# Optimization experiments

Hardware: AMD Instinct MI355X
Metric: run time of the kernel (lower is better)

## Reference

```python
import jax, jax.numpy as jnp
import numpy as np

D = 128; H = 8; DH = D // H; L = 3
NA = 8000; NL = 32000; N = NA + NL
E1 = 65536; D_RPE = 5; D_FFN = 2 * D; RF_H = 128


def _ln(x, eps=1e-5):
    mu = x.mean(-1, keepdims=True)
    var = ((x - mu) ** 2).mean(-1, keepdims=True)
    return (x - mu) * jax.lax.rsqrt(var + eps)


def _rms(x, eps=1e-8):
    rms = jnp.sqrt((x ** 2).sum(-1, keepdims=True)) / np.sqrt(x.shape[-1]).astype(np.float32)
    return x / (rms + eps)


def _seg_softmax(logits, idx, n):
    m = jax.ops.segment_max(logits, idx, num_segments=n)
    e = jnp.exp(logits - m[idx])
    s = jax.ops.segment_sum(e, idx, num_segments=n)
    return e / (s[idx] + 1e-16)


def _gat_layer(x, edge_attr, src, dst, mp_W, mp_b, eu_W, eu_b, Wq, Wk, Wv, Wo, fW1, fb1, fW2, fb2):
    E = src.shape[0]
    # build_mem: gather endpoints, project, LN, ReLU
    cat = jnp.concatenate([x[dst], x[src], edge_attr], axis=-1)       # [E, 3D]
    mem = jax.nn.relu(_ln(cat @ mp_W.T + mp_b))                       # [E, D]
    delta = jax.nn.relu(_ln(mem @ eu_W.T + eu_b))                     # edge_update_block
    edge_attr = _ln(edge_attr + delta)                                # edge_norm
    # multi-head edge attention: q from receiver node, k/v from mem
    q = (x[dst] @ Wq.T).reshape(E, H, DH)
    k = (mem @ Wk.T).reshape(E, H, DH)
    v = (mem @ Wv.T).reshape(E, H, DH)
    logits = (q * k).sum(-1) / np.sqrt(DH).astype(np.float32)         # [E, H]
    attn = _seg_softmax(logits, dst, N)                               # segment softmax over receivers
    msg = (attn[..., None] * v).reshape(E, D) @ Wo.T                  # [E, D]
    aggr = jax.ops.segment_sum(msg, dst, num_segments=N)              # scatter-add
    x = _ln(x + aggr)
    h = jax.nn.relu(x @ fW1.T + fb1) @ fW2.T + fb2
    x = _ln(x + h)
    return x, edge_attr


def _ddc(x_cur, prev_list, W1, b1, W2, b2):
    xs = jnp.stack(prev_list, axis=1)                                 # [N, k, D]
    a = jax.nn.gelu(_rms(x_cur) @ W1.T + b1, approximate=False)
    a = jax.nn.softmax(a @ W2.T + b2, axis=-1)                        # [N, k]
    return (a[..., None] * xs).sum(1)


def setup_inputs() -> dict:
    key = jax.random.key(0)
    ks = iter(jax.random.split(key, 48))
    def nrm(shape, fan_in):
        return jax.random.normal(next(ks), shape, jnp.float32) * np.float32(1.0 / np.sqrt(fan_in))
    inp = {}
    inp['actors'] = jax.random.normal(next(ks), (NA, D), jnp.float32)
    inp['lanes'] = jax.random.normal(next(ks), (NL, D), jnp.float32)
    inp['a2a_attr'] = jax.random.normal(next(ks), (E1, D), jnp.float32)
    inp['l2l_attr'] = jax.random.normal(next(ks), (E1, D), jnp.float32)
    inp['a2l_rpe'] = jax.random.normal(next(ks), (E1, D_RPE), jnp.float32)
    inp['rpe_W'] = nrm((D, D_RPE), D_RPE); inp['rpe_b'] = jnp.zeros((D,), jnp.float32)
    inp['mp_W'] = nrm((L, D, 3 * D), 3 * D); inp['mp_b'] = jnp.zeros((L, D), jnp.float32)
    inp['eu_W'] = nrm((L, D, D), D); inp['eu_b'] = jnp.zeros((L, D), jnp.float32)
    inp['Wq'] = nrm((L, D, D), D); inp['Wk'] = nrm((L, D, D), D)
    inp['Wv'] = nrm((L, D, D), D); inp['Wo'] = nrm((L, D, D), D)
    inp['ffn_W1'] = nrm((L, D_FFN, D), D); inp['ffn_b1'] = jnp.zeros((L, D_FFN), jnp.float32)
    inp['ffn_W2'] = nrm((L, D, D_FFN), D_FFN); inp['ffn_b2'] = jnp.zeros((L, D), jnp.float32)
    inp['rf0_W1'] = nrm((RF_H, D), D); inp['rf0_b1'] = jnp.zeros((RF_H,), jnp.float32)
    inp['rf0_W2'] = nrm((1, RF_H), RF_H); inp['rf0_b2'] = jnp.zeros((1,), jnp.float32)
    inp['rf1_W1'] = nrm((RF_H, D), D); inp['rf1_b1'] = jnp.zeros((RF_H,), jnp.float32)
    inp['rf1_W2'] = nrm((2, RF_H), RF_H); inp['rf1_b2'] = jnp.zeros((2,), jnp.float32)
    inp['a2a_edges'] = jax.random.randint(next(ks), (2, E1), 0, N, jnp.int32)
    inp['l2l_edges'] = jax.random.randint(next(ks), (2, E1), 0, N, jnp.int32)
    inp['a2l_edges'] = jax.random.randint(next(ks), (2, E1), 0, N, jnp.int32)
    return inp


def reference(actors, lanes, a2a_attr, l2l_attr, a2l_rpe, rpe_W, rpe_b,
              mp_W, mp_b, eu_W, eu_b, Wq, Wk, Wv, Wo,
              ffn_W1, ffn_b1, ffn_W2, ffn_b2,
              rf0_W1, rf0_b1, rf0_W2, rf0_b2,
              rf1_W1, rf1_b1, rf1_W2, rf1_b2,
              a2a_edges, l2l_edges, a2l_edges):
    token = jnp.concatenate([actors, lanes], axis=0)                  # single scene: actors then lanes
    edge_index = jnp.concatenate([a2a_edges, l2l_edges, a2l_edges], axis=1)
    a2l_attr = jax.nn.relu(_ln(a2l_rpe @ rpe_W.T + rpe_b))            # proj_a2l_l2a_rpe
    edge_attr = jnp.concatenate([a2a_attr, l2l_attr, a2l_attr], axis=0)
    src, dst = edge_index[0], edge_index[1]
    rf = [(rf0_W1, rf0_b1, rf0_W2, rf0_b2), (rf1_W1, rf1_b1, rf1_W2, rf1_b2)]
    token_list = [token]
    for i in range(L):
        token, edge_attr = _gat_layer(token, edge_attr, src, dst,
                                      mp_W[i], mp_b[i], eu_W[i], eu_b[i],
                                      Wq[i], Wk[i], Wv[i], Wo[i],
                                      ffn_W1[i], ffn_b1[i], ffn_W2[i], ffn_b2[i])
        if i < L - 1:
            token = _ddc(token, token_list, *rf[i])
        token_list.append(token)
    return token[:NA], token[NA:]
```

## Files before the change

kernel.cpp:

```cpp
#include <hip/hip_runtime.h>
#include <hip/hip_bf16.h>

using bf16 = __hip_bfloat16;
typedef __bf16 bf16x8 __attribute__((ext_vector_type(8)));
typedef float f32x4 __attribute__((ext_vector_type(4)));

constexpr int DD   = 128;
constexpr int NACT = 8000;
constexpr int NN   = 40000;
constexpr int E1   = 65536;
constexpr int EE   = 3 * E1;

#define BM 128

__device__ __forceinline__ void gload16(const void* g, void* l) {
  __builtin_amdgcn_global_load_lds((const __attribute__((address_space(1))) void*)g,
                                   (__attribute__((address_space(3))) void*)l, 16, 0, 0);
}

__device__ __forceinline__ int edge_dst(int e, const int* e0, const int* e1, const int* e2) {
  int ty = e >> 16, idx = e & 65535;
  const int* ep = (ty == 0) ? e0 : ((ty == 1) ? e1 : e2);
  return ep[E1 + idx];
}
__device__ __forceinline__ int edge_src(int e, const int* e0, const int* e1, const int* e2) {
  int ty = e >> 16, idx = e & 65535;
  const int* ep = (ty == 0) ? e0 : ((ty == 1) ? e1 : e2);
  return ep[idx];
}

__device__ __forceinline__ void mfma_step(const bf16* A0, int lda, const bf16* B0, int ldb,
                                          f32x4 acc[4][4], int wm, int wn, int lane) {
  const int lr = lane & 15;
  const int lk = (lane >> 4) * 8;
  bf16x8 a[4], b[4];
#pragma unroll
  for (int i = 0; i < 4; i++)
    a[i] = *(const bf16x8*)(A0 + (size_t)(wm * 64 + i * 16 + lr) * lda + lk);
#pragma unroll
  for (int j = 0; j < 4; j++)
    b[j] = *(const bf16x8*)(B0 + (size_t)(wn * 64 + j * 16 + lr) * ldb + lk);
#pragma unroll
  for (int i = 0; i < 4; i++)
#pragma unroll
    for (int j = 0; j < 4; j++)
      acc[i][j] = __builtin_amdgcn_mfma_f32_16x16x32_bf16(a[i], b[j], acc[i][j], 0, 0, 0);
}

__device__ __forceinline__ void mfma_swz(const bf16* A0, const bf16* B0,
                                         f32x4 acc[4][4], int wm, int wn, int lane) {
  const int lr = lane & 15;
  const int g  = lane >> 4;
  const int sw = (g ^ ((lr >> 1) & 3)) * 8;
  bf16x8 a[4], b[4];
#pragma unroll
  for (int i = 0; i < 4; i++)
    a[i] = *(const bf16x8*)(A0 + (wm * 64 + i * 16 + lr) * 32 + sw);
#pragma unroll
  for (int j = 0; j < 4; j++)
    b[j] = *(const bf16x8*)(B0 + (wn * 64 + j * 16 + lr) * 32 + sw);
#pragma unroll
  for (int i = 0; i < 4; i++)
#pragma unroll
    for (int j = 0; j < 4; j++)
      acc[i][j] = __builtin_amdgcn_mfma_f32_16x16x32_bf16(a[i], b[j], acc[i][j], 0, 0, 0);
}

__device__ __forceinline__ void mfma_mixed(const bf16* Am, int lda, const bf16* B0,
                                           f32x4 acc[4][4], int wm, int wn, int lane) {
  const int lr = lane & 15;
  const int g  = lane >> 4;
  const int sw = (g ^ ((lr >> 1) & 3)) * 8;
  bf16x8 a[4], b[4];
#pragma unroll
  for (int i = 0; i < 4; i++)
    a[i] = *(const bf16x8*)(Am + (size_t)(wm * 64 + i * 16 + lr) * lda + g * 8);
#pragma unroll
  for (int j = 0; j < 4; j++)
    b[j] = *(const bf16x8*)(B0 + (wn * 64 + j * 16 + lr) * 32 + sw);
#pragma unroll
  for (int i = 0; i < 4; i++)
#pragma unroll
    for (int j = 0; j < 4; j++)
      acc[i][j] = __builtin_amdgcn_mfma_f32_16x16x32_bf16(a[i], b[j], acc[i][j], 0, 0, 0);
}

__device__ __forceinline__ void row_ln_stats(const f32x4 acc[4][4], float* red_s,
                                             float* red_q, int wm, int wn, int lane) {
  const int lr = lane & 15, lg = lane >> 4;
#pragma unroll
  for (int i = 0; i < 4; i++) {
#pragma unroll
    for (int q = 0; q < 4; q++) {
      float s = acc[i][0][q] + acc[i][1][q] + acc[i][2][q] + acc[i][3][q];
      float t = acc[i][0][q] * acc[i][0][q] + acc[i][1][q] * acc[i][1][q]
              + acc[i][2][q] * acc[i][2][q] + acc[i][3][q] * acc[i][3][q];
#pragma unroll
      for (int off = 1; off < 16; off <<= 1) {
        s += __shfl_xor(s, off);
        t += __shfl_xor(t, off);
      }
      if (lr == 0) {
        int row = wm * 64 + i * 16 + lg * 4 + q;
        red_s[wn * 128 + row] = s;
        red_q[wn * 128 + row] = t;
      }
    }
  }
}

template<int LAST>
__global__ __launch_bounds__(256, 3) void k_fused(
    const bf16* __restrict__ Wmp, const bf16* __restrict__ W2,
    const float* __restrict__ mpb, const float* __restrict__ eub,
    bf16* eah, const bf16* __restrict__ x0h,
    const bf16* __restrict__ qh, bf16* vout,
    float* __restrict__ logi, unsigned* __restrict__ nmax,
    const int* __restrict__ e0, const int* __restrict__ e1, const int* __restrict__ e2)
{
  __shared__ __align__(16) char smem[46080];
  bf16* const mem_s = (bf16*)smem;
  bf16* const Bs2   = (bf16*)(smem + 34816);
  float* const red_s = (float*)(smem + 43008);
  float* const red_q = (float*)(smem + 44032);
  int* const sdst = (int*)(smem + 45056);
  int* const ssrc = (int*)(smem + 45568);

  const int tid = threadIdx.x;
  const int bm0 = blockIdx.x * BM;
  const int lane = tid & 63, w = tid >> 6, wm = w >> 1, wn = w & 1;
  const int swzE = ((lane & 3) ^ ((lane >> 3) & 3)) * 8;

  if (tid < 128) sdst[tid] = edge_dst(bm0 + tid, e0, e1, e2);
  else           ssrc[tid - 128] = edge_src(bm0 + tid - 128, e0, e1, e2);
  __syncthreads();
  const int mr0 = w * 16 + (lane >> 2), mr1 = 64 + w * 16 + (lane >> 2);
  const int rd0 = sdst[mr0], rd1 = sdst[mr1];
  const int rs0 = ssrc[mr0], rs1 = ssrc[mr1];
  const bf16* pd0 = x0h + (size_t)rd0 * DD + swzE;
  const bf16* pd1 = x0h + (size_t)rd1 * DD + swzE;
  const bf16* ps0 = x0h + (size_t)rs0 * DD + swzE;
  const bf16* ps1 = x0h + (size_t)rs1 * DD + swzE;
  const bf16* pe0 = eah + (size_t)(bm0 + mr0) * DD + swzE;
  const bf16* pe1 = eah + (size_t)(bm0 + mr1) * DD + swzE;
  const bf16* pB0 = Wmp + (size_t)mr0 * 384 + swzE;
  const bf16* pB1 = Wmp + (size_t)mr1 * 384 + swzE;
  const bf16* pW20 = W2 + (size_t)mr0 * DD + swzE;
  const bf16* pW21 = W2 + (size_t)mr1 * DD + swzE;

  auto STAGE1 = [&](int kb, int buf) {
    const bf16 *a0, *a1;
    const int k4 = (kb & 3) * 32;
    if (kb < 4)      { a0 = pd0 + k4; a1 = pd1 + k4; }
    else if (kb < 8) { a0 = ps0 + k4; a1 = ps1 + k4; }
    else             { a0 = pe0 + k4; a1 = pe1 + k4; }
    gload16(a0, smem + buf * 8192 + w * 1024);
    gload16(a1, smem + buf * 8192 + 4096 + w * 1024);
    gload16(pB0 + kb * 32, smem + 16384 + buf * 8192 + w * 1024);
    gload16(pB1 + kb * 32, smem + 16384 + buf * 8192 + 4096 + w * 1024);
  };

  f32x4 acc[4][4] = {};
  STAGE1(0, 0);
  __syncthreads();
  int buf = 0;
#pragma unroll
  for (int kb = 0; kb < 12; kb++) {
    if (kb < 11) STAGE1(kb + 1, buf ^ 1);
    mfma_swz((const bf16*)(smem + buf * 8192), (const bf16*)(smem + 16384 + buf * 8192),
             acc, wm, wn, lane);
    __syncthreads();
    buf ^= 1;
  }

  const int lr = lane & 15, lg = lane >> 4;
  const int colb = wn * 64 + lr;
  const int rowb = wm * 64 + lg * 4;

#pragma unroll
  for (int j = 0; j < 4; j++) {
    float bj = mpb[colb + j * 16];
#pragma unroll
    for (int i = 0; i < 4; i++)
#pragma unroll
      for (int q = 0; q < 4; q++) acc[i][j][q] += bj;
  }
  row_ln_stats(acc, red_s, red_q, wm, wn, lane);
  __syncthreads();
#pragma unroll
  for (int i = 0; i < 4; i++) {
#pragma unroll
    for (int q = 0; q < 4; q++) {
      int row = rowb + i * 16 + q;
      float Sm = red_s[row] + red_s[128 + row];
      float Qs = red_q[row] + red_q[128 + row];
      float mu = Sm * 0.0078125f;
      float var = Qs * 0.0078125f - mu * mu;
      float inv = 1.0f / sqrtf(var + 1e-5f);
#pragma unroll
      for (int j = 0; j < 4; j++)
        mem_s[row * 136 + colb + j * 16] =
            __float2bfloat16(fmaxf((acc[i][j][q] - mu) * inv, 0.f));
    }
  }

  auto GEMM2 = [&](int voff, f32x4 a2[4][4]) {
#pragma unroll 1
    for (int kb = 0; kb < 4; kb++) {
      __syncthreads();
      gload16(pW20 + voff + kb * 32, smem + 34816 + w * 1024);
      gload16(pW21 + voff + kb * 32, smem + 34816 + 4096 + w * 1024);
      __syncthreads();
      mfma_mixed(mem_s + kb * 32, 136, Bs2, a2, wm, wn, lane);
    }
  };
  auto store_tile = [&](bf16* dst) {
#pragma unroll
    for (int c = 0; c < 8; c++) {
      int off = c * 2048 + tid * 8;
      int row = off >> 7, col = off & 127;
      *(uint4*)(dst + (size_t)bm0 * DD + off) = *(uint4*)&mem_s[row * 136 + col];
    }
  };

  if constexpr (LAST == 0) {
    f32x4 acc2[4][4] = {};
    GEMM2(0, acc2);
#pragma unroll
    for (int j = 0; j < 4; j++) {
      float bj = eub[colb + j * 16];
#pragma unroll
      for (int i = 0; i < 4; i++)
#pragma unroll
        for (int q = 0; q < 4; q++) acc2[i][j][q] += bj;
    }
    __syncthreads();
    row_ln_stats(acc2, red_s, red_q, wm, wn, lane);
    __syncthreads();
#pragma unroll
    for (int i = 0; i < 4; i++) {
#pragma unroll
      for (int q = 0; q < 4; q++) {
        int row = rowb + i * 16 + q;
        float Sm = red_s[row] + red_s[128 + row];
        float Qs = red_q[row] + red_q[128 + row];
        float mu = Sm * 0.0078125f;
        float var = Qs * 0.0078125f - mu * mu;
        float inv = 1.0f / sqrtf(var + 1e-5f);
        int r = bm0 + row;
#pragma unroll
        for (int j = 0; j < 4; j++) {
          float d = fmaxf((acc2[i][j][q] - mu) * inv, 0.f);
          float eo = __bfloat162float(eah[(size_t)r * DD + colb + j * 16]);
          acc2[i][j][q] = eo + d;
        }
      }
    }
    __syncthreads();
    row_ln_stats(acc2, red_s, red_q, wm, wn, lane);
    __syncthreads();
#pragma unroll
    for (int i = 0; i < 4; i++) {
#pragma unroll
      for (int q = 0; q < 4; q++) {
        int row = rowb + i * 16 + q;
        float Sm = red_s[row] + red_s[128 + row];
        float Qs = red_q[row] + red_q[128 + row];
        float mu = Sm * 0.0078125f;
        float var = Qs * 0.0078125f - mu * mu;
        float inv = 1.0f / sqrtf(var + 1e-5f);
#pragma unroll
        for (int j = 0; j < 4; j++)
          mem_s[row * 136 + colb + j * 16] =
              __float2bfloat16((acc2[i][j][q] - mu) * inv);
      }
    }
    __syncthreads();
    store_tile(eah);
  } else {
    f32x4 acc2[4][4] = {};
    GEMM2(0, acc2);
#pragma unroll
    for (int i = 0; i < 4; i++) {
#pragma unroll
      for (int q = 0; q < 4; q++) {
        int row = rowb + i * 16 + q;
        int dst = sdst[row];
#pragma unroll
        for (int j = 0; j < 4; j++) {
          int h = wn * 4 + j;
          float qv = __bfloat162float(qh[(size_t)dst * DD + h * 16 + lr]);
          float p = acc2[i][j][q] * qv;
#pragma unroll
          for (int off = 1; off < 16; off <<= 1) p += __shfl_xor(p, off);
          if (lr == 0) {
            p *= 0.25f;
            int e = bm0 + row;
            logi[(size_t)e * 8 + h] = p;
            unsigned u = __float_as_uint(p);
            u = (u & 0x80000000u) ? ~u : (u | 0x80000000u);
            atomicMax(nmax + (size_t)dst * 8 + h, u);
          }
        }
      }
    }
    f32x4 acc3[4][4] = {};
    GEMM2(128 * DD, acc3);
    __syncthreads();
#pragma unroll
    for (int i = 0; i < 4; i++)
#pragma unroll
      for (int q = 0; q < 4; q++) {
        int row = rowb + i * 16 + q;
#pragma unroll
        for (int j = 0; j < 4; j++)
          mem_s[row * 136 + colb + j * 16] = __float2bfloat16(acc3[i][j][q]);
      }
    __syncthreads();
    store_tile(vout);
  }
}

template<int EPI>
__global__ __launch_bounds__(256, 3) void k_gemmG(
    const bf16* __restrict__ A, const bf16* __restrict__ B, void* __restrict__ out,
    const float* __restrict__ bias, const float* __restrict__ aux,
    int M, int K, int lda, int ldc)
{
  __shared__ __align__(16) char smem[36864];
  bf16* const stg = (bf16*)smem;
  float* const red_s = (float*)(smem + 34816);
  float* const red_q = (float*)(smem + 35840);

  const int tid = threadIdx.x, lane = tid & 63, w = tid >> 6;
  const int wm = w >> 1, wn = w & 1;
  const int bm0 = blockIdx.x * BM, bn0 = blockIdx.y * BM;
  const int swzE = ((lane & 3) ^ ((lane >> 3) & 3)) * 8;

  const bf16* pA[2];
  const bf16* pB[2];
#pragma unroll
  for (int r = 0; r < 2; r++) {
    int ra = bm0 + r * 64 + w * 16 + (lane >> 2);
    if (ra > M - 1) ra = M - 1;
    pA[r] = A + (size_t)ra * lda + swzE;
    pB[r] = B + (size_t)(bn0 + r * 64 + w * 16 + (lane >> 2)) * K + swzE;
  }
  auto STAGE = [&](int kb, int buf) {
#pragma unroll
    for (int r = 0; r < 2; r++) {
      gload16(pA[r] + kb * 32, smem + buf * 8192 + r * 4096 + w * 1024);
      gload16(pB[r] + kb * 32, smem + 16384 + buf * 8192 + r * 4096 + w * 1024);
    }
  };

  f32x4 acc[4][4] = {};
  const int KB = K >> 5;
  STAGE(0, 0);
  __syncthreads();
  int buf = 0;
#pragma unroll 1
  for (int kb = 0; kb < KB; kb++) {
    if (kb + 1 < KB) STAGE(kb + 1, buf ^ 1);
    mfma_swz((const bf16*)(smem + buf * 8192), (const bf16*)(smem + 16384 + buf * 8192),
             acc, wm, wn, lane);
    __syncthreads();
    buf ^= 1;
  }

  const int lr = lane & 15, lg = lane >> 4;
  const int colb = wn * 64 + lr;
  const int rowb = wm * 64 + lg * 4;

  if constexpr (EPI == 1 || EPI == 5) {
    if constexpr (EPI == 5) {
#pragma unroll
      for (int j = 0; j < 4; j++) {
        float b = bias[bn0 + colb + j * 16];
#pragma unroll
        for (int i = 0; i < 4; i++)
#pragma unroll
          for (int q = 0; q < 4; q++) acc[i][j][q] = fmaxf(acc[i][j][q] + b, 0.f);
      }
    }
#pragma unroll
    for (int i = 0; i < 4; i++)
#pragma unroll
      for (int q = 0; q < 4; q++) {
        int row = rowb + i * 16 + q;
#pragma unroll
        for (int j = 0; j < 4; j++)
          stg[row * 136 + colb + j * 16] = __float2bfloat16(acc[i][j][q]);
      }
    __syncthreads();
#pragma unroll
    for (int c = 0; c < 8; c++) {
      int off = c * 2048 + tid * 8;
      int row = off >> 7, col = off & 127;
      int r = bm0 + row;
      if (r < M)
        *(uint4*)((bf16*)out + (size_t)r * ldc + bn0 + col) = *(uint4*)&stg[row * 136 + col];
    }
  }

  if constexpr (EPI == 6) {
#pragma unroll
    for (int i = 0; i < 4; i++)
#pragma unroll
      for (int q = 0; q < 4; q++) {
        int r = bm0 + rowb + i * 16 + q;
        if (r < M) {
#pragma unroll
          for (int j = 0; j < 4; j++)
            acc[i][j][q] += bias[colb + j * 16] + aux[(size_t)r * DD + colb + j * 16];
        }
      }
    row_ln_stats(acc, red_s, red_q, wm, wn, lane);
    __syncthreads();
    float* const fstg = (float*)smem;
#pragma unroll
    for (int h = 0; h < 2; h++) {
      if (wm == h) {
#pragma unroll
        for (int i = 0; i < 4; i++)
#pragma unroll
          for (int q = 0; q < 4; q++) {
            int row = rowb + i * 16 + q;
            float Sm = red_s[row] + red_s[128 + row];
            float Qs = red_q[row] + red_q[128 + row];
            float mu = Sm * 0.0078125f;
            float var = Qs * 0.0078125f - mu * mu;
            float inv = 1.0f / sqrtf(var + 1e-5f);
            int rloc = row - h * 64;
#pragma unroll
            for (int j = 0; j < 4; j++)
              fstg[rloc * 132 + colb + j * 16] = (acc[i][j][q] - mu) * inv;
          }
      }
      __syncthreads();
#pragma unroll
      for (int c = 0; c < 8; c++) {
        int boff = c * 4096 + tid * 16;
        int row = boff >> 9, col = (boff & 511) >> 2;
        int r = bm0 + h * 64 + row;
        if (r < M)
          *(float4*)((float*)out + (size_t)r * DD + col) = *(float4*)&fstg[row * 132 + col];
      }
      __syncthreads();
    }
  }
}

__global__ __launch_bounds__(256) void k_msg(
    const bf16* __restrict__ Vh, const bf16* __restrict__ Wo,
    float* __restrict__ aggr, const float* __restrict__ att,
    const int* __restrict__ e0, const int* __restrict__ e1, const int* __restrict__ e2)
{
  __shared__ __align__(16) bf16 As[128 * 40];
  __shared__ __align__(16) bf16 Bs[128 * 40];
  const int tid = threadIdx.x, lane = tid & 63, w = tid >> 6, wm = w >> 1, wn = w & 1;
  const int bm0 = blockIdx.x * BM;
  f32x4 acc[4][4] = {};
#pragma unroll 1
  for (int kb = 0; kb < 4; kb++) {
    const int k0 = kb * 32;
    for (int c = tid; c < 512; c += 256) {
      int row = c >> 2, c8 = (c & 3) * 8;
      int e = bm0 + row;
      uint4 v = *(const uint4*)(Vh + (size_t)e * DD + k0 + c8);
      float at = att[(size_t)e * 8 + ((k0 + c8) >> 4)];
      union { uint4 u; bf16 hh[8]; } vv; vv.u = v;
#pragma unroll
      for (int t = 0; t < 8; t++)
        vv.hh[t] = __float2bfloat16(at * __bfloat162float(vv.hh[t]));
      *(uint4*)&As[row * 40 + c8] = vv.u;
      *(uint4*)&Bs[row * 40 + c8] = *(const uint4*)(Wo + (size_t)row * DD + k0 + c8);
    }
    __syncthreads();
    mfma_step(As, 40, Bs, 40, acc, wm, wn, lane);
    __syncthreads();
  }
  const int lr = lane & 15, lg = lane >> 4;
  const int colb = wn * 64 + lr;
  const int rowb = wm * 64 + lg * 4;
#pragma unroll
  for (int i = 0; i < 4; i++)
#pragma unroll
    for (int q = 0; q < 4; q++) {
      int e = bm0 + rowb + i * 16 + q;
      int dst = edge_dst(e, e0, e1, e2);
#pragma unroll
      for (int j = 0; j < 4; j++)
        atomicAdd(aggr + (size_t)dst * DD + colb + j * 16, acc[i][j][q]);
    }
}

__device__ __forceinline__ float2 ln_pair(float2 v, float eps) {
  float s = v.x + v.y, sq = v.x * v.x + v.y * v.y;
#pragma unroll
  for (int o = 32; o > 0; o >>= 1) {
    s += __shfl_xor(s, o);
    sq += __shfl_xor(sq, o);
  }
  float mu = s * 0.0078125f;
  float var = sq * 0.0078125f - mu * mu;
  float inv = 1.0f / sqrtf(var + eps);
  return make_float2((v.x - mu) * inv, (v.y - mu) * inv);
}

__global__ void k_init_ea(const float* __restrict__ a2a, const float* __restrict__ l2l,
                          const float* __restrict__ rpe, const float* __restrict__ rpeW,
                          const float* __restrict__ rpeb, bf16* __restrict__ eah) {
  int r = blockIdx.x * 4 + (threadIdx.x >> 6);
  int lane = threadIdx.x & 63;
  int ty = r >> 16, idx = r & 65535;
  int c0 = lane * 2;
  float2 y;
  if (ty < 2) {
    y = *(const float2*)((ty == 0 ? a2a : l2l) + (size_t)idx * DD + c0);
  } else {
    float rp0 = rpe[idx * 5 + 0], rp1 = rpe[idx * 5 + 1], rp2 = rpe[idx * 5 + 2];
    float rp3 = rpe[idx * 5 + 3], rp4 = rpe[idx * 5 + 4];
    float2 v;
    v.x = rpeb[c0]     + rp0 * rpeW[c0 * 5]           + rp1 * rpeW[c0 * 5 + 1]
        + rp2 * rpeW[c0 * 5 + 2]     + rp3 * rpeW[c0 * 5 + 3]     + rp4 * rpeW[c0 * 5 + 4];
    v.y = rpeb[c0 + 1] + rp0 * rpeW[(c0 + 1) * 5]     + rp1 * rpeW[(c0 + 1) * 5 + 1]
        + rp2 * rpeW[(c0 + 1) * 5 + 2] + rp3 * rpeW[(c0 + 1) * 5 + 3] + rp4 * rpeW[(c0 + 1) * 5 + 4];
    y = ln_pair(v, 1e-5f);
    y.x = fmaxf(y.x, 0.f);
    y.y = fmaxf(y.y, 0.f);
  }
  size_t o = (size_t)r * DD + c0;
  eah[o] = __float2bfloat16(y.x);
  eah[o + 1] = __float2bfloat16(y.y);
}

__global__ void k_x1(const float* __restrict__ actors, const float* __restrict__ lanesp,
                     const float* __restrict__ aggr, float* __restrict__ x1,
                     bf16* __restrict__ x1h, int R) {
  int r = blockIdx.x * 4 + (threadIdx.x >> 6);
  if (r >= R) return;
  int lane = threadIdx.x & 63;
  int c0 = lane * 2;
  const float* xp = (r < NACT) ? (actors + (size_t)r * DD) : (lanesp + (size_t)(r - NACT) * DD);
  float2 v = *(const float2*)(xp + c0);
  float2 a = *(const float2*)(aggr + (size_t)r * DD + c0);
  v.x += a.x; v.y += a.y;
  float2 y = ln_pair(v, 1e-5f);
  size_t o = (size_t)r * DD + c0;
  *(float2*)(x1 + o) = y;
  x1h[o] = __float2bfloat16(y.x);
  x1h[o + 1] = __float2bfloat16(y.y);
}

__global__ void k_evals(float* __restrict__ logit, const unsigned* __restrict__ nmax,
                        float* __restrict__ nsum,
                        const int* __restrict__ e0, const int* __restrict__ e1,
                        const int* __restrict__ e2) {
  int gid = blockIdx.x * 256 + threadIdx.x;
  int e = gid >> 3, h = gid & 7;
  int dst = edge_dst(e, e0, e1, e2);
  unsigned u = nmax[(size_t)dst * 8 + h];
  float m = (u & 0x80000000u) ? __uint_as_float(u ^ 0x80000000u) : __uint_as_float(~u);
  float v = expf(logit[gid] - m);
  logit[gid] = v;
  atomicAdd(nsum + (size_t)dst * 8 + h, v);
}

__global__ void k_attn(float* __restrict__ logit, const float* __restrict__ nsum,
                       const int* __restrict__ e0, const int* __restrict__ e1,
                       const int* __restrict__ e2) {
  int gid = blockIdx.x * 256 + threadIdx.x;
  int e = gid >> 3, h = gid & 7;
  int dst = edge_dst(e, e0, e1, e2);
  logit[gid] = logit[gid] / (nsum[(size_t)dst * 8 + h] + 1e-16f);
}

__global__ void k_conv(const float* __restrict__ a, bf16* __restrict__ b, int n) {
  int i = blockIdx.x * 256 + threadIdx.x;
  if (i < n) b[i] = __float2bfloat16(a[i]);
}

__global__ void k_x0h(const float* __restrict__ actors, const float* __restrict__ lanesp,
                      bf16* __restrict__ x0h) {
  int gid = blockIdx.x * 256 + threadIdx.x;
  int n = gid >> 7, c = gid & 127;
  float v = (n < NACT) ? actors[(size_t)n * DD + c] : lanesp[(size_t)(n - NACT) * DD + c];
  x0h[gid] = __float2bfloat16(v);
}

extern "C" void kernel_launch(void* const* d_in, const int* in_sizes, int n_in,
                              void* d_out, int out_size, void* d_ws, size_t ws_size,
                              hipStream_t stream) {
  (void)in_sizes; (void)n_in; (void)out_size;
  if (ws_size < (128ull << 20)) return;

  const float* actors = (const float*)d_in[0];
  const float* lanesp = (const float*)d_in[1];
  const float* a2a    = (const float*)d_in[2];
  const float* l2l    = (const float*)d_in[3];
  const float* rpe    = (const float*)d_in[4];
  const float* rpeW   = (const float*)d_in[5];
  const float* rpeb   = (const float*)d_in[6];
  const float* mpW    = (const float*)d_in[7];
  const float* mpb    = (const float*)d_in[8];
  const float* euW    = (const float*)d_in[9];
  const float* eub    = (const float*)d_in[10];
  const float* Wq     = (const float*)d_in[11];
  const float* Wk     = (const float*)d_in[12];
  const float* Wv     = (const float*)d_in[13];
  const float* Wo     = (const float*)d_in[14];
  const float* fW1    = (const float*)d_in[15];
  const float* fb1    = (const float*)d_in[16];
  const float* fW2    = (const float*)d_in[17];
  const float* fb2    = (const float*)d_in[18];
  const int* e0 = (const int*)d_in[27];
  const int* e1 = (const int*)d_in[28];
  const int* e2 = (const int*)d_in[29];

  char* ws = (char*)d_ws;
  bf16* W_MP = (bf16*)ws;
  bf16* W_EU = W_MP + 147456;
  bf16* W_WQ = W_EU + 32768;
  bf16* W_KV = W_WQ + 16384;
  bf16* W_WO = W_KV + 32768;
  bf16* W_F1 = W_WO + 16384;
  bf16* W_F2 = W_F1 + 32768;

  bf16*  X0H = (bf16*)(ws + (1ull << 20));
  bf16*  QH  = (bf16*)(ws + (12ull << 20));
  float* POOL = (float*)(ws + (24ull << 20));
  float*    AGGR = POOL;
  float*    X1   = POOL + 5120000;
  float*    LOGI = POOL + 10240000;
  unsigned* NMAX = (unsigned*)(POOL + 11812864);
  float*    NSUM = POOL + 12132864;
  bf16* EAH = (bf16*)(ws + (80ull << 20));
  bf16* VH  = EAH;
  bf16* X1H = X0H;
  bf16* H1H = EAH;

  k_conv<<<576, 256, 0, stream>>>(mpW, W_MP, 147456);
  k_conv<<<128, 256, 0, stream>>>(euW, W_EU, 32768);
  k_conv<<<64, 256, 0, stream>>>(Wq + 2 * 16384, W_WQ, 16384);
  k_conv<<<64, 256, 0, stream>>>(Wk + 2 * 16384, W_KV, 16384);
  k_conv<<<64, 256, 0, stream>>>(Wv + 2 * 16384, W_KV + 16384, 16384);
  k_conv<<<64, 256, 0, stream>>>(Wo + 2 * 16384, W_WO, 16384);
  k_conv<<<128, 256, 0, stream>>>(fW1 + 2 * 32768, W_F1, 32768);
  k_conv<<<128, 256, 0, stream>>>(fW2 + 2 * 32768, W_F2, 32768);
  k_x0h<<<20000, 256, 0, stream>>>(actors, lanesp, X0H);
  k_init_ea<<<49152, 256, 0, stream>>>(a2a, l2l, rpe, rpeW, rpeb, EAH);

  k_gemmG<1><<<313, 256, 0, stream>>>(X0H, W_WQ, QH, nullptr, nullptr, NN, 128, 128, DD);

  hipMemsetAsync(AGGR, 0, (size_t)NN * DD * 4, stream);
  hipMemsetAsync(NMAX, 0, (size_t)NN * 8 * 4, stream);
  hipMemsetAsync(NSUM, 0, (size_t)NN * 8 * 4, stream);

  for (int i = 0; i < 2; i++) {
    k_fused<0><<<EE / BM, 256, 0, stream>>>(W_MP + i * 49152, W_EU + i * 16384,
        mpb + i * 128, eub + i * 128, EAH, X0H, nullptr, nullptr,
        nullptr, nullptr, e0, e1, e2);
  }
  k_fused<1><<<EE / BM, 256, 0, stream>>>(W_MP + 2 * 49152, W_KV,
      mpb + 2 * 128, nullptr, EAH, X0H, QH, VH, LOGI, NMAX, e0, e1, e2);

  k_evals<<<EE * 8 / 256, 256, 0, stream>>>(LOGI, NMAX, NSUM, e0, e1, e2);
  k_attn<<<EE * 8 / 256, 256, 0, stream>>>(LOGI, NSUM, e0, e1, e2);

  k_msg<<<EE / BM, 256, 0, stream>>>(VH, W_WO, AGGR, LOGI, e0, e1, e2);

  k_x1<<<NN / 4, 256, 0, stream>>>(actors, lanesp, AGGR, X1, X1H, NN);
  k_gemmG<5><<<dim3(313, 2), 256, 0, stream>>>(X1H, W_F1, H1H, fb1 + 2 * 256, nullptr,
                                               NN, 128, 128, 256);
  k_gemmG<6><<<dim3(313, 1), 256, 0, stream>>>(H1H, W_F2, d_out, fb2 + 2 * 128, X1,
                                               NN, 256, 256, DD);
}
```

Baseline: 529.9 us.

## Fuse all three edge layers and edge-attr init into one persistent-tile kernel

Merges edge-attribute initialization and the three per-layer edge kernels into a single kernel. Each block keeps its 128-edge tile's edge attributes on-chip (registers plus LDS) across layers, so the bf16 edge-attr array is no longer written and re-read through global memory between layers. The mp GEMM now reads gathered node rows and weights directly from global memory rather than through the double-buffered async LDS pipeline. Separately, the softmax normalization kernel is removed by folding the division by the segment sum into the message kernel. The trade-offs are higher register pressure, loss of the LDS prefetch pipeline for the gathers, and fewer but longer kernels.

```diff
diff --git a/kernel.cpp b/kernel.cpp
--- a/kernel.cpp
+++ b/kernel.cpp
@@ -12,6 +12,8 @@
 constexpr int EE   = 3 * E1;
 
 #define BM 128
+#define LDK 36
+#define LDT 136
 
 __device__ __forceinline__ void gload16(const void* g, void* l) {
   __builtin_amdgcn_global_load_lds((const __attribute__((address_space(1))) void*)g,
@@ -27,6 +29,15 @@
   int ty = e >> 16, idx = e & 65535;
   const int* ep = (ty == 0) ? e0 : ((ty == 1) ? e1 : e2);
   return ep[idx];
+}
+
+__device__ __forceinline__ unsigned short bfbits(float f) {
+  bf16 h = __float2bfloat16(f);
+  return __builtin_bit_cast(unsigned short, h);
+}
+__device__ __forceinline__ float bffloat(unsigned short u) {
+  bf16 h = __builtin_bit_cast(bf16, u);
+  return __bfloat162float(h);
 }
 
 __device__ __forceinline__ void mfma_step(const bf16* A0, int lda, const bf16* B0, int ldb,
@@ -66,25 +77,6 @@
       acc[i][j] = __builtin_amdgcn_mfma_f32_16x16x32_bf16(a[i], b[j], acc[i][j], 0, 0, 0);
 }
 
-__device__ __forceinline__ void mfma_mixed(const bf16* Am, int lda, const bf16* B0,
-                                           f32x4 acc[4][4], int wm, int wn, int lane) {
-  const int lr = lane & 15;
-  const int g  = lane >> 4;
-  const int sw = (g ^ ((lr >> 1) & 3)) * 8;
-  bf16x8 a[4], b[4];
-#pragma unroll
-  for (int i = 0; i < 4; i++)
-    a[i] = *(const bf16x8*)(Am + (size_t)(wm * 64 + i * 16 + lr) * lda + g * 8);
-#pragma unroll
-  for (int j = 0; j < 4; j++)
-    b[j] = *(const bf16x8*)(B0 + (wn * 64 + j * 16 + lr) * 32 + sw);
-#pragma unroll
-  for (int i = 0; i < 4; i++)
-#pragma unroll
-    for (int j = 0; j < 4; j++)
-      acc[i][j] = __builtin_amdgcn_mfma_f32_16x16x32_bf16(a[i], b[j], acc[i][j], 0, 0, 0);
-}
-
 __device__ __forceinline__ void row_ln_stats(const f32x4 acc[4][4], float* red_s,
                                              float* red_q, int wm, int wn, int lane) {
   const int lr = lane & 15, lg = lane >> 4;
@@ -109,179 +101,260 @@
   }
 }
 
-template<int LAST>
-__global__ __launch_bounds__(256, 3) void k_fused(
-    const bf16* __restrict__ Wmp, const bf16* __restrict__ W2,
+__device__ __forceinline__ float2 ln_pair(float2 v, float eps) {
+  float s = v.x + v.y, sq = v.x * v.x + v.y * v.y;
+#pragma unroll
+  for (int o = 32; o > 0; o >>= 1) {
+    s += __shfl_xor(s, o);
+    sq += __shfl_xor(sq, o);
+  }
+  float mu = s * 0.0078125f;
+  float var = sq * 0.0078125f - mu * mu;
+  float inv = 1.0f / sqrtf(var + eps);
+  return make_float2((v.x - mu) * inv, (v.y - mu) * inv);
+}
+
+__global__ __launch_bounds__(256, 3) void k_edge(
+    const bf16* __restrict__ WMP, const bf16* __restrict__ WEU, const bf16* __restrict__ WKV,
     const float* __restrict__ mpb, const float* __restrict__ eub,
-    bf16* eah, const bf16* __restrict__ x0h,
-    const bf16* __restrict__ qh, bf16* vout,
-    float* __restrict__ logi, unsigned* __restrict__ nmax,
+    const float* __restrict__ a2a, const float* __restrict__ l2l,
+    const float* __restrict__ rpe, const float* __restrict__ rpeW,
+    const float* __restrict__ rpeb,
+    const bf16* __restrict__ x0h, const bf16* __restrict__ qh,
+    bf16* __restrict__ vout, float* __restrict__ logi, unsigned* __restrict__ nmax,
     const int* __restrict__ e0, const int* __restrict__ e1, const int* __restrict__ e2)
 {
-  __shared__ __align__(16) char smem[46080];
-  bf16* const mem_s = (bf16*)smem;
-  bf16* const Bs2   = (bf16*)(smem + 34816);
-  float* const red_s = (float*)(smem + 43008);
-  float* const red_q = (float*)(smem + 44032);
-  int* const sdst = (int*)(smem + 45056);
-  int* const ssrc = (int*)(smem + 45568);
+  __shared__ __align__(16) bf16 tile[128 * LDT];
+  __shared__ float red_s[256], red_q[256];
+  __shared__ int sdst[128], ssrc[128];
 
   const int tid = threadIdx.x;
   const int bm0 = blockIdx.x * BM;
   const int lane = tid & 63, w = tid >> 6, wm = w >> 1, wn = w & 1;
-  const int swzE = ((lane & 3) ^ ((lane >> 3) & 3)) * 8;
+  const int lr = lane & 15, g = lane >> 4;
+  const int colb = wn * 64 + lr;
+  const int rowb = wm * 64 + g * 4;
 
   if (tid < 128) sdst[tid] = edge_dst(bm0 + tid, e0, e1, e2);
   else           ssrc[tid - 128] = edge_src(bm0 + tid - 128, e0, e1, e2);
+
+  const int ty = bm0 >> 16, idx0 = bm0 & 65535;
+  if (ty < 2) {
+    const float* src = (ty == 0 ? a2a : l2l) + (size_t)idx0 * DD;
+#pragma unroll
+    for (int c = 0; c < 16; c++) {
+      int off = c * 1024 + tid * 4;
+      int row = off >> 7, col = off & 127;
+      float4 v = *(const float4*)(src + off);
+      ushort4 h;
+      h.x = bfbits(v.x); h.y = bfbits(v.y); h.z = bfbits(v.z); h.w = bfbits(v.w);
+      *(ushort4*)&tile[row * LDT + col] = h;
+    }
+  } else {
+    int c0 = lane * 2;
+#pragma unroll 1
+    for (int rr = 0; rr < 32; rr++) {
+      int r = w * 32 + rr;
+      const float* rp = rpe + (size_t)(idx0 + r) * 5;
+      float r0 = rp[0], r1 = rp[1], r2 = rp[2], r3 = rp[3], r4 = rp[4];
+      float2 v;
+      v.x = rpeb[c0] + r0 * rpeW[c0 * 5] + r1 * rpeW[c0 * 5 + 1] + r2 * rpeW[c0 * 5 + 2]
+          + r3 * rpeW[c0 * 5 + 3] + r4 * rpeW[c0 * 5 + 4];
+      v.y = rpeb[c0 + 1] + r0 * rpeW[(c0 + 1) * 5] + r1 * rpeW[(c0 + 1) * 5 + 1]
+          + r2 * rpeW[(c0 + 1) * 5 + 2] + r3 * rpeW[(c0 + 1) * 5 + 3] + r4 * rpeW[(c0 + 1) * 5 + 4];
+      float2 y = ln_pair(v, 1e-5f);
+      tile[r * LDT + c0]     = __float2bfloat16(fmaxf(y.x, 0.f));
+      tile[r * LDT + c0 + 1] = __float2bfloat16(fmaxf(y.y, 0.f));
+    }
+  }
   __syncthreads();
-  const int mr0 = w * 16 + (lane >> 2), mr1 = 64 + w * 16 + (lane >> 2);
-  const int rd0 = sdst[mr0], rd1 = sdst[mr1];
-  const int rs0 = ssrc[mr0], rs1 = ssrc[mr1];
-  const bf16* pd0 = x0h + (size_t)rd0 * DD + swzE;
-  const bf16* pd1 = x0h + (size_t)rd1 * DD + swzE;
-  const bf16* ps0 = x0h + (size_t)rs0 * DD + swzE;
-  const bf16* ps1 = x0h + (size_t)rs1 * DD + swzE;
-  const bf16* pe0 = eah + (size_t)(bm0 + mr0) * DD + swzE;
-  const bf16* pe1 = eah + (size_t)(bm0 + mr1) * DD + swzE;
-  const bf16* pB0 = Wmp + (size_t)mr0 * 384 + swzE;
-  const bf16* pB1 = Wmp + (size_t)mr1 * 384 + swzE;
-  const bf16* pW20 = W2 + (size_t)mr0 * DD + swzE;
-  const bf16* pW21 = W2 + (size_t)mr1 * DD + swzE;
-
-  auto STAGE1 = [&](int kb, int buf) {
-    const bf16 *a0, *a1;
-    const int k4 = (kb & 3) * 32;
-    if (kb < 4)      { a0 = pd0 + k4; a1 = pd1 + k4; }
-    else if (kb < 8) { a0 = ps0 + k4; a1 = ps1 + k4; }
-    else             { a0 = pe0 + k4; a1 = pe1 + k4; }
-    gload16(a0, smem + buf * 8192 + w * 1024);
-    gload16(a1, smem + buf * 8192 + 4096 + w * 1024);
-    gload16(pB0 + kb * 32, smem + 16384 + buf * 8192 + w * 1024);
-    gload16(pB1 + kb * 32, smem + 16384 + buf * 8192 + 4096 + w * 1024);
+
+  int an[4], as_[4];
+#pragma unroll
+  for (int i = 0; i < 4; i++) {
+    int ar = wm * 64 + i * 16 + lr;
+    an[i] = sdst[ar];
+    as_[i] = ssrc[ar];
+  }
+
+  unsigned pk[4][4][2];
+
+  auto GEMM1 = [&](const bf16* Wm, f32x4 (&A)[4][4]) {
+#pragma unroll
+    for (int kb = 0; kb < 12; kb++) {
+      bf16x8 a[4], b[4];
+#pragma unroll
+      for (int j = 0; j < 4; j++)
+        b[j] = *(const bf16x8*)(Wm + (size_t)(wn * 64 + j * 16 + lr) * 384 + kb * 32 + g * 8);
+#pragma unroll
+      for (int i = 0; i < 4; i++) {
+        if (kb < 4)
+          a[i] = *(const bf16x8*)(x0h + (size_t)an[i] * DD + kb * 32 + g * 8);
+        else if (kb < 8)
+          a[i] = *(const bf16x8*)(x0h + (size_t)as_[i] * DD + (kb - 4) * 32 + g * 8);
+        else
+          a[i] = *(const bf16x8*)(tile + (wm * 64 + i * 16 + lr) * LDT + (kb - 8) * 32 + g * 8);
+      }
+      __builtin_amdgcn_s_setprio(1);
+#pragma unroll
+      for (int i = 0; i < 4; i++)
+#pragma unroll
+        for (int j = 0; j < 4; j++)
+          A[i][j] = __builtin_amdgcn_mfma_f32_16x16x32_bf16(a[i], b[j], A[i][j], 0, 0, 0);
+      __builtin_amdgcn_s_setprio(0);
+    }
   };
 
-  f32x4 acc[4][4] = {};
-  STAGE1(0, 0);
-  __syncthreads();
-  int buf = 0;
-#pragma unroll
-  for (int kb = 0; kb < 12; kb++) {
-    if (kb < 11) STAGE1(kb + 1, buf ^ 1);
-    mfma_swz((const bf16*)(smem + buf * 8192), (const bf16*)(smem + 16384 + buf * 8192),
-             acc, wm, wn, lane);
-    __syncthreads();
-    buf ^= 1;
-  }
-
-  const int lr = lane & 15, lg = lane >> 4;
-  const int colb = wn * 64 + lr;
-  const int rowb = wm * 64 + lg * 4;
-
-#pragma unroll
-  for (int j = 0; j < 4; j++) {
-    float bj = mpb[colb + j * 16];
+  auto GEMM2 = [&](const bf16* W2, f32x4 (&A)[4][4]) {
+#pragma unroll
+    for (int kb = 0; kb < 4; kb++) {
+      bf16x8 a[4], b[4];
+#pragma unroll
+      for (int j = 0; j < 4; j++)
+        b[j] = *(const bf16x8*)(W2 + (size_t)(wn * 64 + j * 16 + lr) * DD + kb * 32 + g * 8);
+#pragma unroll
+      for (int i = 0; i < 4; i++)
+        a[i] = *(const bf16x8*)(tile + (wm * 64 + i * 16 + lr) * LDT + kb * 32 + g * 8);
+      __builtin_amdgcn_s_setprio(1);
+#pragma unroll
+      for (int i = 0; i < 4; i++)
+#pragma unroll
+        for (int j = 0; j < 4; j++)
+          A[i][j] = __builtin_amdgcn_mfma_f32_16x16x32_bf16(a[i], b[j], A[i][j], 0, 0, 0);
+      __builtin_amdgcn_s_setprio(0);
+    }
+  };
+
+  auto ln_mi = [&](int row, float& mu, float& inv) {
+    float Sm = red_s[row] + red_s[128 + row];
+    float Qs = red_q[row] + red_q[128 + row];
+    mu = Sm * 0.0078125f;
+    float var = Qs * 0.0078125f - mu * mu;
+    inv = 1.0f / sqrtf(var + 1e-5f);
+  };
+
+  auto EPI1 = [&](const float* bias, f32x4 (&A)[4][4]) {
+#pragma unroll
+    for (int j = 0; j < 4; j++) {
+      float bj = bias[colb + j * 16];
+#pragma unroll
+      for (int i = 0; i < 4; i++)
+#pragma unroll
+        for (int q = 0; q < 4; q++) A[i][j][q] += bj;
+    }
+    row_ln_stats(A, red_s, red_q, wm, wn, lane);
+    __syncthreads();
 #pragma unroll
     for (int i = 0; i < 4; i++)
-#pragma unroll
-      for (int q = 0; q < 4; q++) acc[i][j][q] += bj;
-  }
-  row_ln_stats(acc, red_s, red_q, wm, wn, lane);
-  __syncthreads();
-#pragma unroll
-  for (int i = 0; i < 4; i++) {
-#pragma unroll
-    for (int q = 0; q < 4; q++) {
-      int row = rowb + i * 16 + q;
-      float Sm = red_s[row] + red_s[128 + row];
-      float Qs = red_q[row] + red_q[128 + row];
-      float mu = Sm * 0.0078125f;
-      float var = Qs * 0.0078125f - mu * mu;
-      float inv = 1.0f / sqrtf(var + 1e-5f);
-#pragma unroll
-      for (int j = 0; j < 4; j++)
-        mem_s[row * 136 + colb + j * 16] =
-            __float2bfloat16(fmaxf((acc[i][j][q] - mu) * inv, 0.f));
-    }
-  }
-
-  auto GEMM2 = [&](int voff, f32x4 a2[4][4]) {
-#pragma unroll 1
-    for (int kb = 0; kb < 4; kb++) {
-      __syncthreads();
-      gload16(pW20 + voff + kb * 32, smem + 34816 + w * 1024);
-      gload16(pW21 + voff + kb * 32, smem + 34816 + 4096 + w * 1024);
-      __syncthreads();
-      mfma_mixed(mem_s + kb * 32, 136, Bs2, a2, wm, wn, lane);
-    }
-  };
-  auto store_tile = [&](bf16* dst) {
-#pragma unroll
-    for (int c = 0; c < 8; c++) {
-      int off = c * 2048 + tid * 8;
-      int row = off >> 7, col = off & 127;
-      *(uint4*)(dst + (size_t)bm0 * DD + off) = *(uint4*)&mem_s[row * 136 + col];
-    }
-  };
-
-  if constexpr (LAST == 0) {
-    f32x4 acc2[4][4] = {};
-    GEMM2(0, acc2);
-#pragma unroll
-    for (int j = 0; j < 4; j++) {
-      float bj = eub[colb + j * 16];
-#pragma unroll
-      for (int i = 0; i < 4; i++)
-#pragma unroll
-        for (int q = 0; q < 4; q++) acc2[i][j][q] += bj;
-    }
-    __syncthreads();
-    row_ln_stats(acc2, red_s, red_q, wm, wn, lane);
-    __syncthreads();
-#pragma unroll
-    for (int i = 0; i < 4; i++) {
 #pragma unroll
       for (int q = 0; q < 4; q++) {
         int row = rowb + i * 16 + q;
-        float Sm = red_s[row] + red_s[128 + row];
-        float Qs = red_q[row] + red_q[128 + row];
-        float mu = Sm * 0.0078125f;
-        float var = Qs * 0.0078125f - mu * mu;
-        float inv = 1.0f / sqrtf(var + 1e-5f);
-        int r = bm0 + row;
-#pragma unroll
-        for (int j = 0; j < 4; j++) {
-          float d = fmaxf((acc2[i][j][q] - mu) * inv, 0.f);
-          float eo = __bfloat162float(eah[(size_t)r * DD + colb + j * 16]);
-          acc2[i][j][q] = eo + d;
-        }
-      }
-    }
-    __syncthreads();
-    row_ln_stats(acc2, red_s, red_q, wm, wn, lane);
-    __syncthreads();
-#pragma unroll
-    for (int i = 0; i < 4; i++) {
+        float mu, inv;
+        ln_mi(row, mu, inv);
+#pragma unroll
+        for (int j = 0; j < 4; j++)
+          tile[row * LDT + colb + j * 16] =
+              __float2bfloat16(fmaxf((A[i][j][q] - mu) * inv, 0.f));
+      }
+    __syncthreads();
+  };
+
+  auto EPI2 = [&](const float* bias, f32x4 (&A)[4][4]) {
+#pragma unroll
+    for (int j = 0; j < 4; j++) {
+      float bj = bias[colb + j * 16];
+#pragma unroll
+      for (int i = 0; i < 4; i++)
+#pragma unroll
+        for (int q = 0; q < 4; q++) A[i][j][q] += bj;
+    }
+    row_ln_stats(A, red_s, red_q, wm, wn, lane);
+    __syncthreads();
+#pragma unroll
+    for (int i = 0; i < 4; i++)
 #pragma unroll
       for (int q = 0; q < 4; q++) {
         int row = rowb + i * 16 + q;
-        float Sm = red_s[row] + red_s[128 + row];
-        float Qs = red_q[row] + red_q[128 + row];
-        float mu = Sm * 0.0078125f;
-        float var = Qs * 0.0078125f - mu * mu;
-        float inv = 1.0f / sqrtf(var + 1e-5f);
-#pragma unroll
-        for (int j = 0; j < 4; j++)
-          mem_s[row * 136 + colb + j * 16] =
-              __float2bfloat16((acc2[i][j][q] - mu) * inv);
-      }
-    }
-    __syncthreads();
-    store_tile(eah);
-  } else {
+        float mu, inv;
+        ln_mi(row, mu, inv);
+#pragma unroll
+        for (int jp = 0; jp < 2; jp++) {
+          unsigned u = pk[i][q][jp];
+          float d0 = fmaxf((A[i][2 * jp][q] - mu) * inv, 0.f);
+          float d1 = fmaxf((A[i][2 * jp + 1][q] - mu) * inv, 0.f);
+          A[i][2 * jp][q]     = bffloat((unsigned short)(u & 0xffffu)) + d0;
+          A[i][2 * jp + 1][q] = bffloat((unsigned short)(u >> 16)) + d1;
+        }
+      }
+    __syncthreads();
+    row_ln_stats(A, red_s, red_q, wm, wn, lane);
+    __syncthreads();
+#pragma unroll
+    for (int i = 0; i < 4; i++)
+#pragma unroll
+      for (int q = 0; q < 4; q++) {
+        int row = rowb + i * 16 + q;
+        float mu, inv;
+        ln_mi(row, mu, inv);
+#pragma unroll
+        for (int jp = 0; jp < 2; jp++) {
+          unsigned lo = bfbits((A[i][2 * jp][q] - mu) * inv);
+          unsigned hi = bfbits((A[i][2 * jp + 1][q] - mu) * inv);
+          pk[i][q][jp] = lo | (hi << 16);
+        }
+      }
+  };
+
+  auto SCATTER = [&]() {
+    unsigned short* tw = (unsigned short*)tile;
+#pragma unroll
+    for (int i = 0; i < 4; i++)
+#pragma unroll
+      for (int q = 0; q < 4; q++) {
+        int base = (rowb + i * 16 + q) * LDT + colb;
+#pragma unroll
+        for (int jp = 0; jp < 2; jp++) {
+          unsigned u = pk[i][q][jp];
+          tw[base + jp * 32]      = (unsigned short)(u & 0xffffu);
+          tw[base + jp * 32 + 16] = (unsigned short)(u >> 16);
+        }
+      }
+    __syncthreads();
+  };
+
+#pragma unroll 1
+  for (int l = 0; l < 2; l++) {
+    if (l) SCATTER();
+    f32x4 acc[4][4] = {};
+    GEMM1(WMP + l * 49152, acc);
+    if (l == 0) {
+      const unsigned short* tu = (const unsigned short*)tile;
+#pragma unroll
+      for (int i = 0; i < 4; i++)
+#pragma unroll
+        for (int q = 0; q < 4; q++) {
+          int base = (rowb + i * 16 + q) * LDT + colb;
+#pragma unroll
+          for (int jp = 0; jp < 2; jp++)
+            pk[i][q][jp] = (unsigned)tu[base + jp * 32] |
+                           ((unsigned)tu[base + jp * 32 + 16] << 16);
+        }
+    }
+    EPI1(mpb + l * 128, acc);
     f32x4 acc2[4][4] = {};
-    GEMM2(0, acc2);
-#pragma unroll
-    for (int i = 0; i < 4; i++) {
+    GEMM2(WEU + l * 16384, acc2);
+    EPI2(eub + l * 128, acc2);
+  }
+
+  SCATTER();
+  {
+    f32x4 acc[4][4] = {};
+    GEMM1(WMP + 2 * 49152, acc);
+    EPI1(mpb + 2 * 128, acc);
+    f32x4 acc2[4][4] = {};
+    GEMM2(WKV, acc2);
+#pragma unroll
+    for (int i = 0; i < 4; i++)
 #pragma unroll
       for (int q = 0; q < 4; q++) {
         int row = rowb + i * 16 + q;
@@ -303,9 +376,8 @@
           }
         }
       }
-    }
     f32x4 acc3[4][4] = {};
-    GEMM2(128 * DD, acc3);
+    GEMM2(WKV + 16384, acc3);
     __syncthreads();
 #pragma unroll
     for (int i = 0; i < 4; i++)
@@ -314,10 +386,15 @@
         int row = rowb + i * 16 + q;
 #pragma unroll
         for (int j = 0; j < 4; j++)
-          mem_s[row * 136 + colb + j * 16] = __float2bfloat16(acc3[i][j][q]);
-      }
-    __syncthreads();
-    store_tile(vout);
+          tile[row * LDT + colb + j * 16] = __float2bfloat16(acc3[i][j][q]);
+      }
+    __syncthreads();
+#pragma unroll
+    for (int c = 0; c < 8; c++) {
+      int off = c * 2048 + tid * 8;
+      int row = off >> 7, col = off & 127;
+      *(uint4*)(vout + (size_t)bm0 * DD + off) = *(uint4*)&tile[row * LDT + col];
+    }
   }
 }
 
@@ -390,7 +467,7 @@
         int row = rowb + i * 16 + q;
 #pragma unroll
         for (int j = 0; j < 4; j++)
-          stg[row * 136 + colb + j * 16] = __float2bfloat16(acc[i][j][q]);
+          stg[row * LDT + colb + j * 16] = __float2bfloat16(acc[i][j][q]);
       }
     __syncthreads();
 #pragma unroll
@@ -399,7 +476,7 @@
       int row = off >> 7, col = off & 127;
       int r = bm0 + row;
       if (r < M)
-        *(uint4*)((bf16*)out + (size_t)r * ldc + bn0 + col) = *(uint4*)&stg[row * 136 + col];
+        *(uint4*)((bf16*)out + (size_t)r * ldc + bn0 + col) = *(uint4*)&stg[row * LDT + col];
     }
   }
 
@@ -453,13 +530,16 @@
 
 __global__ __launch_bounds__(256) void k_msg(
     const bf16* __restrict__ Vh, const bf16* __restrict__ Wo,
-    float* __restrict__ aggr, const float* __restrict__ att,
+    float* __restrict__ aggr, const float* __restrict__ evals, const float* __restrict__ nsum,
     const int* __restrict__ e0, const int* __restrict__ e1, const int* __restrict__ e2)
 {
   __shared__ __align__(16) bf16 As[128 * 40];
   __shared__ __align__(16) bf16 Bs[128 * 40];
+  __shared__ int sdst[128];
   const int tid = threadIdx.x, lane = tid & 63, w = tid >> 6, wm = w >> 1, wn = w & 1;
   const int bm0 = blockIdx.x * BM;
+  if (tid < 128) sdst[tid] = edge_dst(bm0 + tid, e0, e1, e2);
+  __syncthreads();
   f32x4 acc[4][4] = {};
 #pragma unroll 1
   for (int kb = 0; kb < 4; kb++) {
@@ -467,8 +547,9 @@
     for (int c = tid; c < 512; c += 256) {
       int row = c >> 2, c8 = (c & 3) * 8;
       int e = bm0 + row;
+      int h = (k0 + c8) >> 4;
       uint4 v = *(const uint4*)(Vh + (size_t)e * DD + k0 + c8);
-      float at = att[(size_t)e * 8 + ((k0 + c8) >> 4)];
+      float at = evals[(size_t)e * 8 + h] / (nsum[(size_t)sdst[row] * 8 + h] + 1e-16f);
       union { uint4 u; bf16 hh[8]; } vv; vv.u = v;
 #pragma unroll
       for (int t = 0; t < 8; t++)
@@ -487,52 +568,11 @@
   for (int i = 0; i < 4; i++)
 #pragma unroll
     for (int q = 0; q < 4; q++) {
-      int e = bm0 + rowb + i * 16 + q;
-      int dst = edge_dst(e, e0, e1, e2);
+      int dst = sdst[rowb + i * 16 + q];
 #pragma unroll
       for (int j = 0; j < 4; j++)
         atomicAdd(aggr + (size_t)dst * DD + colb + j * 16, acc[i][j][q]);
     }
-}
-
-__device__ __forceinline__ float2 ln_pair(float2 v, float eps) {
-  float s = v.x + v.y, sq = v.x * v.x + v.y * v.y;
-#pragma unroll
-  for (int o = 32; o > 0; o >>= 1) {
-    s += __shfl_xor(s, o);
-    sq += __shfl_xor(sq, o);
-  }
-  float mu = s * 0.0078125f;
-  float var = sq * 0.0078125f - mu * mu;
-  float inv = 1.0f / sqrtf(var + eps);
-  return make_float2((v.x - mu) * inv, (v.y - mu) * inv);
-}
-
-__global__ void k_init_ea(const float* __restrict__ a2a, const float* __restrict__ l2l,
-                          const float* __restrict__ rpe, const float* __restrict__ rpeW,
-                          const float* __restrict__ rpeb, bf16* __restrict__ eah) {
-  int r = blockIdx.x * 4 + (threadIdx.x >> 6);
-  int lane = threadIdx.x & 63;
-  int ty = r >> 16, idx = r & 65535;
-  int c0 = lane * 2;
-  float2 y;
-  if (ty < 2) {
-    y = *(const float2*)((ty == 0 ? a2a : l2l) + (size_t)idx * DD + c0);
-  } else {
-    float rp0 = rpe[idx * 5 + 0], rp1 = rpe[idx * 5 + 1], rp2 = rpe[idx * 5 + 2];
-    float rp3 = rpe[idx * 5 + 3], rp4 = rpe[idx * 5 + 4];
-    float2 v;
-    v.x = rpeb[c0]     + rp0 * rpeW[c0 * 5]           + rp1 * rpeW[c0 * 5 + 1]
-        + rp2 * rpeW[c0 * 5 + 2]     + rp3 * rpeW[c0 * 5 + 3]     + rp4 * rpeW[c0 * 5 + 4];
-    v.y = rpeb[c0 + 1] + rp0 * rpeW[(c0 + 1) * 5]     + rp1 * rpeW[(c0 + 1) * 5 + 1]
-        + rp2 * rpeW[(c0 + 1) * 5 + 2] + rp3 * rpeW[(c0 + 1) * 5 + 3] + rp4 * rpeW[(c0 + 1) * 5 + 4];
-    y = ln_pair(v, 1e-5f);
-    y.x = fmaxf(y.x, 0.f);
-    y.y = fmaxf(y.y, 0.f);
-  }
-  size_t o = (size_t)r * DD + c0;
-  eah[o] = __float2bfloat16(y.x);
-  eah[o + 1] = __float2bfloat16(y.y);
 }
 
 __global__ void k_x1(const float* __restrict__ actors, const float* __restrict__ lanesp,
@@ -565,15 +605,6 @@
   float v = expf(logit[gid] - m);
   logit[gid] = v;
   atomicAdd(nsum + (size_t)dst * 8 + h, v);
-}
-
-__global__ void k_attn(float* __restrict__ logit, const float* __restrict__ nsum,
-                       const int* __restrict__ e0, const int* __restrict__ e1,
-                       const int* __restrict__ e2) {
-  int gid = blockIdx.x * 256 + threadIdx.x;
-  int e = gid >> 3, h = gid & 7;
-  int dst = edge_dst(e, e0, e1, e2);
-  logit[gid] = logit[gid] / (nsum[(size_t)dst * 8 + h] + 1e-16f);
 }
 
 __global__ void k_conv(const float* __restrict__ a, bf16* __restrict__ b, int n) {
@@ -635,10 +666,9 @@
   float*    LOGI = POOL + 10240000;
   unsigned* NMAX = (unsigned*)(POOL + 11812864);
   float*    NSUM = POOL + 12132864;
-  bf16* EAH = (bf16*)(ws + (80ull << 20));
-  bf16* VH  = EAH;
+  bf16* VH  = (bf16*)(ws + (80ull << 20));
   bf16* X1H = X0H;
-  bf16* H1H = EAH;
+  bf16* H1H = VH;
 
   k_conv<<<576, 256, 0, stream>>>(mpW, W_MP, 147456);
   k_conv<<<128, 256, 0, stream>>>(euW, W_EU, 32768);
@@ -649,7 +679,6 @@
   k_conv<<<128, 256, 0, stream>>>(fW1 + 2 * 32768, W_F1, 32768);
   k_conv<<<128, 256, 0, stream>>>(fW2 + 2 * 32768, W_F2, 32768);
   k_x0h<<<20000, 256, 0, stream>>>(actors, lanesp, X0H);
-  k_init_ea<<<49152, 256, 0, stream>>>(a2a, l2l, rpe, rpeW, rpeb, EAH);
 
   k_gemmG<1><<<313, 256, 0, stream>>>(X0H, W_WQ, QH, nullptr, nullptr, NN, 128, 128, DD);
 
@@ -657,18 +686,13 @@
   hipMemsetAsync(NMAX, 0, (size_t)NN * 8 * 4, stream);
   hipMemsetAsync(NSUM, 0, (size_t)NN * 8 * 4, stream);
 
-  for (int i = 0; i < 2; i++) {
-    k_fused<0><<<EE / BM, 256, 0, stream>>>(W_MP + i * 49152, W_EU + i * 16384,
-        mpb + i * 128, eub + i * 128, EAH, X0H, nullptr, nullptr,
-        nullptr, nullptr, e0, e1, e2);
-  }
-  k_fused<1><<<EE / BM, 256, 0, stream>>>(W_MP + 2 * 49152, W_KV,
-      mpb + 2 * 128, nullptr, EAH, X0H, QH, VH, LOGI, NMAX, e0, e1, e2);
+  k_edge<<<EE / BM, 256, 0, stream>>>(W_MP, W_EU, W_KV, mpb, eub,
+                                      a2a, l2l, rpe, rpeW, rpeb,
+                                      X0H, QH, VH, LOGI, NMAX, e0, e1, e2);
 
   k_evals<<<EE * 8 / 256, 256, 0, stream>>>(LOGI, NMAX, NSUM, e0, e1, e2);
-  k_attn<<<EE * 8 / 256, 256, 0, stream>>>(LOGI, NSUM, e0, e1, e2);
-
-  k_msg<<<EE / BM, 256, 0, stream>>>(VH, W_WO, AGGR, LOGI, e0, e1, e2);
+
+  k_msg<<<EE / BM, 256, 0, stream>>>(VH, W_WO, AGGR, LOGI, NSUM, e0, e1, e2);
 
   k_x1<<<NN / 4, 256, 0, stream>>>(actors, lanesp, AGGR, X1, X1H, NN);
   k_gemmG<5><<<dim3(313, 2), 256, 0, stream>>>(X1H, W_F1, H1H, fb1 + 2 * 256, nullptr,
```

Measured after the change: 663.1 us. 25.1% more time.
